# Kernel tuning notes

Measured on AMD Instinct MI355X. Metric: run time of the kernel, lower is better.

Reference implementation:

```python
import jax, jax.numpy as jnp
import numpy as np

B, C_IN, H, W = 4, 256, 200, 176
A = 6            # anchors per location (3 sizes x 2 rotations)
NUM_CLS = 4      # 3 classes + background
K = 100
N_ANCH = A * H * W


def setup_inputs() -> dict:
    key = jax.random.key(0)
    k1, k2, k3, k4, k5, k6 = jax.random.split(key, 6)
    x = jax.random.normal(k1, (B, C_IN, H, W), dtype=jnp.float32)
    scale = 1.0 / np.sqrt(C_IN)
    cls_w = jax.random.normal(k2, (NUM_CLS * A, C_IN), dtype=jnp.float32) * scale
    cls_b = jnp.zeros((NUM_CLS * A,), dtype=jnp.float32)
    reg_w = jax.random.normal(k3, (7 * A, C_IN), dtype=jnp.float32) * scale * 0.1
    reg_b = jnp.zeros((7 * A,), dtype=jnp.float32)
    # anchors: [N,7] = (x, y, z, dx, dy, dz, ry) with strictly positive sizes
    xyz = jax.random.uniform(k4, (N_ANCH, 3), minval=-35.0, maxval=35.0)
    sizes = jax.random.uniform(k5, (N_ANCH, 3), minval=1.0, maxval=4.0)
    rot = jax.random.uniform(k6, (N_ANCH, 1), minval=-np.pi, maxval=np.pi)
    anchors = jnp.concatenate([xyz, sizes, rot], axis=-1).astype(jnp.float32)
    return {"x": x, "cls_w": cls_w, "cls_b": cls_b,
            "reg_w": reg_w, "reg_b": reg_b, "anchors": anchors}


def _decode(deltas, anchors):
    # SECOND-style residual box decoder.  deltas, anchors: [B, N, 7]
    xa, ya, za, dxa, dya, dza, ra = jnp.split(anchors, 7, axis=-1)
    xt, yt, zt, dxt, dyt, dzt, rt = jnp.split(deltas, 7, axis=-1)
    diag = jnp.sqrt(dxa * dxa + dya * dya)
    xg = xt * diag + xa
    yg = yt * diag + ya
    zg = zt * dza + za
    dxg = jnp.exp(dxt) * dxa
    dyg = jnp.exp(dyt) * dya
    dzg = jnp.exp(dzt) * dza
    rg = rt + ra
    return jnp.concatenate([xg, yg, zg, dxg, dyg, dzg, rg], axis=-1)


def reference(x, cls_w, cls_b, reg_w, reg_b, anchors):
    # 1x1 conv heads: [B,C_in,H,W] -> [B,C_out,H,W]
    cls_pred = jnp.einsum('bchw,oc->bohw', x, cls_w) + cls_b[None, :, None, None]
    reg_pred = jnp.einsum('bchw,oc->bohw', x, reg_w) + reg_b[None, :, None, None]
    # permute(0,2,3,1).reshape(B, num_anchors, -1)
    cls_pred = jnp.transpose(cls_pred, (0, 2, 3, 1)).reshape(B, N_ANCH, NUM_CLS)
    reg_pred = jnp.transpose(reg_pred, (0, 2, 3, 1)).reshape(B, N_ANCH, 7)
    batch_anchors = jnp.broadcast_to(anchors[None], (B, N_ANCH, 7))
    pred_bboxes = _decode(reg_pred, batch_anchors)
    pred_scores = jax.nn.softmax(cls_pred, axis=-1)
    # per-frame top-k over max foreground score (classes 1:)
    max_scores = jnp.max(pred_scores[..., 1:], axis=-1)      # [B, N]
    _, topk_inds = jax.lax.top_k(max_scores, K)              # [B, K]
    topk_bboxes = jnp.take_along_axis(pred_bboxes, topk_inds[..., None], axis=1)
    topk_scores = jnp.take_along_axis(pred_scores, topk_inds[..., None], axis=1)
    return (topk_scores, topk_bboxes)
```

## Files before the change

### kernel.cpp

```cpp
#include <hip/hip_runtime.h>

#define BB 4
#define CIN 256
#define HW 35200
#define AA 6
#define NANCH (AA * HW)
#define TOPK 100
#define NBIN 4096
#define BINBASE 28416
#define CAP 4096
#define SMAX 4096
#define TILES 138

__device__ __forceinline__ unsigned sbin(unsigned bits) {
  int v = (int)(bits >> 15) - BINBASE;
  v = v < 0 ? 0 : v;
  v = v > (NBIN - 1) ? (NBIN - 1) : v;
  return (unsigned)v;
}

__device__ __forceinline__ float sc4(float4 l) {
  float m = fmaxf(fmaxf(l.x, l.y), fmaxf(l.z, l.w));
  float e0 = expf(l.x - m), e1 = expf(l.y - m);
  float e2 = expf(l.z - m), e3 = expf(l.w - m);
  return fmaxf(fmaxf(e1, e2), e3) / (e0 + e1 + e2 + e3);
}

#define FMA4(A, W, S)                                      \
  A.x = fmaf(S, W.x, A.x); A.y = fmaf(S, W.y, A.y);        \
  A.z = fmaf(S, W.z, A.z); A.w = fmaf(S, W.w, A.w);

__global__ __launch_bounds__(256, 4) void k1_scores(
    const float* __restrict__ x, const float* __restrict__ cls_w,
    const float* __restrict__ cls_b, unsigned int* __restrict__ hist,
    float* __restrict__ maxsc) {
  int bid = blockIdx.x;
  int b = bid / TILES, tile = bid % TILES;
  int tid = threadIdx.x;

  __shared__ __align__(16) float swf[CIN * 24];
  __shared__ unsigned lh[NBIN];
  for (int i = tid; i < CIN * 24; i += 256)
    swf[(i % CIN) * 24 + (i / CIN)] = cls_w[i];
  for (int i = tid; i < NBIN; i += 256) lh[i] = 0;
  __syncthreads();
  const float4* sw4 = (const float4*)swf;

  int hwg = tile * 256 + tid;
  bool act = hwg < HW;
  int hwc = act ? hwg : (HW - 1);
  const float* xb = x + (size_t)b * CIN * HW + hwc;

  float4 a0 = make_float4(cls_b[0], cls_b[1], cls_b[2], cls_b[3]);
  float4 a1 = make_float4(cls_b[4], cls_b[5], cls_b[6], cls_b[7]);
  float4 a2 = make_float4(cls_b[8], cls_b[9], cls_b[10], cls_b[11]);
  float4 a3 = make_float4(cls_b[12], cls_b[13], cls_b[14], cls_b[15]);
  float4 a4 = make_float4(cls_b[16], cls_b[17], cls_b[18], cls_b[19]);
  float4 a5 = make_float4(cls_b[20], cls_b[21], cls_b[22], cls_b[23]);

#pragma unroll 8
  for (int c = 0; c < CIN; ++c) {
    float xv = xb[(size_t)c * HW];
    const float4* wr = sw4 + c * 6;
    float4 w0 = wr[0], w1 = wr[1], w2 = wr[2];
    float4 w3 = wr[3], w4 = wr[4], w5 = wr[5];
    FMA4(a0, w0, xv) FMA4(a1, w1, xv) FMA4(a2, w2, xv)
    FMA4(a3, w3, xv) FMA4(a4, w4, xv) FMA4(a5, w5, xv)
  }

  if (act) {
    float s0 = sc4(a0), s1 = sc4(a1), s2 = sc4(a2);
    float s3 = sc4(a3), s4 = sc4(a4), s5 = sc4(a5);
    float* mp = maxsc + (size_t)b * NANCH + (size_t)hwg * 6u;
    mp[0] = s0; mp[1] = s1; mp[2] = s2; mp[3] = s3; mp[4] = s4; mp[5] = s5;
    atomicAdd(&lh[sbin(__float_as_uint(s0))], 1u);
    atomicAdd(&lh[sbin(__float_as_uint(s1))], 1u);
    atomicAdd(&lh[sbin(__float_as_uint(s2))], 1u);
    atomicAdd(&lh[sbin(__float_as_uint(s3))], 1u);
    atomicAdd(&lh[sbin(__float_as_uint(s4))], 1u);
    atomicAdd(&lh[sbin(__float_as_uint(s5))], 1u);
  }
  __syncthreads();
  unsigned* gh = hist + (size_t)b * NBIN;
  for (int i = tid; i < NBIN; i += 256) {
    unsigned c = lh[i];
    if (c) atomicAdd(&gh[i], c);
  }
}

__global__ __launch_bounds__(256) void k2_thresh(
    const unsigned int* __restrict__ hist, unsigned int* __restrict__ thresh) {
  int b = blockIdx.x, tid = threadIdx.x;
  const unsigned* h = hist + (size_t)b * NBIN;
  unsigned r[16];
  unsigned s = 0;
#pragma unroll
  for (int i = 0; i < 16; ++i) { r[i] = h[tid * 16 + i]; s += r[i]; }
  __shared__ unsigned seg[256];
  seg[tid] = s;
  __syncthreads();
  for (int d = 1; d < 256; d <<= 1) {
    unsigned add = (tid + d < 256) ? seg[tid + d] : 0u;
    __syncthreads();
    seg[tid] += add;
    __syncthreads();
  }
  unsigned above = (tid < 255) ? seg[tid + 1] : 0u;
  if (above < TOPK && above + s >= TOPK) {
    unsigned c = above, T = 0;
    for (int i = 15; i >= 0; --i) {
      c += r[i];
      if (c >= TOPK) { T = tid * 16u + (unsigned)i; break; }
    }
    thresh[b] = T;
  }
}

__global__ __launch_bounds__(256) void k3_compact(
    const float* __restrict__ maxsc, const unsigned int* __restrict__ thresh,
    unsigned int* __restrict__ cand_count, unsigned long long* __restrict__ cand) {
  unsigned p = blockIdx.x * 256u + threadIdx.x;
  unsigned b = p / NANCH, n = p % NANCH;
  unsigned bits = __float_as_uint(maxsc[p]);
  bool pred = sbin(bits) >= thresh[b];
  unsigned long long mask = __ballot(pred);
  if (mask) {
    int lane = threadIdx.x & 63;
    int leader = (int)__ffsll((unsigned long long)mask) - 1;
    unsigned base = 0;
    if (lane == leader)
      base = atomicAdd(&cand_count[b], (unsigned)__popcll(mask));
    base = __shfl(base, leader, 64);
    if (pred) {
      unsigned pos = base + (unsigned)__popcll(mask & ((1ull << lane) - 1ull));
      if (pos < CAP)
        cand[(size_t)b * CAP + pos] =
            ((unsigned long long)bits << 32) | (unsigned)(~n);
    }
  }
}

__global__ __launch_bounds__(256) void k4_sort(
    const unsigned long long* __restrict__ cand,
    const unsigned int* __restrict__ cand_count, unsigned int* __restrict__ topk) {
  int b = blockIdx.x, tid = threadIdx.x;
  __shared__ unsigned long long sh[SMAX];
  unsigned cnt = cand_count[b];
  if (cnt > CAP) cnt = CAP;
  unsigned S = 128;
  while (S < cnt) S <<= 1;
  for (unsigned t = tid; t < S; t += 256)
    sh[t] = (t < cnt) ? cand[(size_t)b * CAP + t] : 0ULL;
  __syncthreads();
  for (unsigned kk = 2; kk <= S; kk <<= 1) {
    for (unsigned jj = kk >> 1; jj > 0; jj >>= 1) {
      for (unsigned t = tid; t < S; t += 256) {
        unsigned ixj = t ^ jj;
        if (ixj > t) {
          unsigned long long a = sh[t], c = sh[ixj];
          bool sw = ((t & kk) == 0) ? (a < c) : (a > c);
          if (sw) { sh[t] = c; sh[ixj] = a; }
        }
      }
      __syncthreads();
    }
  }
  if (tid < TOPK)
    topk[b * TOPK + tid] = ~(unsigned)(sh[tid] & 0xFFFFFFFFULL);
}

__global__ __launch_bounds__(256) void k5_out(
    const float* __restrict__ x, const float* __restrict__ cls_w,
    const float* __restrict__ cls_b, const float* __restrict__ reg_w,
    const float* __restrict__ reg_b, const float* __restrict__ anchors,
    const unsigned int* __restrict__ topk, float* __restrict__ out) {
  int bk = blockIdx.x;
  int b = bk / TOPK, k = bk % TOPK;
  unsigned n = topk[b * TOPK + k];
  int a = (int)(n % AA);
  unsigned hw = n / AA;
  int tid = threadIdx.x;

  float xv = x[(size_t)b * CIN * HW + (size_t)tid * HW + hw];
  float part[11];
#pragma unroll
  for (int j = 0; j < 4; ++j) part[j] = xv * cls_w[(a * 4 + j) * CIN + tid];
#pragma unroll
  for (int j = 0; j < 7; ++j) part[4 + j] = xv * reg_w[(a * 7 + j) * CIN + tid];

#pragma unroll
  for (int j = 0; j < 11; ++j) {
    float v = part[j];
    for (int off = 32; off > 0; off >>= 1) v += __shfl_down(v, off, 64);
    part[j] = v;
  }
  __shared__ float red[4][11];
  int wave = tid >> 6, lane = tid & 63;
  if (lane == 0) {
#pragma unroll
    for (int j = 0; j < 11; ++j) red[wave][j] = part[j];
  }
  __syncthreads();
  if (tid == 0) {
    float tot[11];
#pragma unroll
    for (int j = 0; j < 11; ++j)
      tot[j] = red[0][j] + red[1][j] + red[2][j] + red[3][j];
    float l0 = tot[0] + cls_b[a * 4 + 0];
    float l1 = tot[1] + cls_b[a * 4 + 1];
    float l2 = tot[2] + cls_b[a * 4 + 2];
    float l3 = tot[3] + cls_b[a * 4 + 3];
    float m = fmaxf(fmaxf(l0, l1), fmaxf(l2, l3));
    float e0 = expf(l0 - m), e1 = expf(l1 - m);
    float e2 = expf(l2 - m), e3 = expf(l3 - m);
    float inv = 1.0f / (e0 + e1 + e2 + e3);
    float* os = out + ((size_t)b * TOPK + k) * 4;
    os[0] = e0 * inv; os[1] = e1 * inv; os[2] = e2 * inv; os[3] = e3 * inv;
    const float* an = anchors + (size_t)n * 7;
    float xa = an[0], ya = an[1], za = an[2];
    float dxa = an[3], dya = an[4], dza = an[5], ra = an[6];
    float xt = tot[4] + reg_b[a * 7 + 0];
    float yt = tot[5] + reg_b[a * 7 + 1];
    float zt = tot[6] + reg_b[a * 7 + 2];
    float dxt = tot[7] + reg_b[a * 7 + 3];
    float dyt = tot[8] + reg_b[a * 7 + 4];
    float dzt = tot[9] + reg_b[a * 7 + 5];
    float rt = tot[10] + reg_b[a * 7 + 6];
    float diag = sqrtf(dxa * dxa + dya * dya);
    float* ob = out + (size_t)BB * TOPK * 4 + ((size_t)b * TOPK + k) * 7;
    ob[0] = xt * diag + xa;
    ob[1] = yt * diag + ya;
    ob[2] = zt * dza + za;
    ob[3] = expf(dxt) * dxa;
    ob[4] = expf(dyt) * dya;
    ob[5] = expf(dzt) * dza;
    ob[6] = rt + ra;
  }
}

extern "C" void kernel_launch(void* const* d_in, const int* in_sizes, int n_in,
                              void* d_out, int out_size, void* d_ws, size_t ws_size,
                              hipStream_t stream) {
  const float* x       = (const float*)d_in[0];
  const float* cls_w   = (const float*)d_in[1];
  const float* cls_b   = (const float*)d_in[2];
  const float* reg_w   = (const float*)d_in[3];
  const float* reg_b   = (const float*)d_in[4];
  const float* anchors = (const float*)d_in[5];
  float* out = (float*)d_out;

  char* ws = (char*)d_ws;
  size_t off = 0;
  unsigned int* hist = (unsigned int*)(ws + off);        off += (size_t)BB * NBIN * 4;
  unsigned int* cand_count = (unsigned int*)(ws + off);  off += 64;
  unsigned int* thresh = (unsigned int*)(ws + off);      off += 64;
  unsigned long long* cand = (unsigned long long*)(ws + off); off += (size_t)BB * CAP * 8;
  unsigned int* topk = (unsigned int*)(ws + off);        off += 2048;
  float* maxsc = (float*)(ws + off);

  hipMemsetAsync(hist, 0, (size_t)BB * NBIN * 4 + 64, stream);

  k1_scores<<<BB * TILES, 256, 0, stream>>>(x, cls_w, cls_b, hist, maxsc);
  k2_thresh<<<BB, 256, 0, stream>>>(hist, thresh);
  k3_compact<<<(BB * NANCH) / 256, 256, 0, stream>>>(maxsc, thresh, cand_count, cand);
  k4_sort<<<BB, 256, 0, stream>>>(cand, cand_count, topk);
  k5_out<<<BB * TOPK, 256, 0, stream>>>(x, cls_w, cls_b, reg_w, reg_b, anchors,
                                        topk, out);
}
```

Before: 277.7 us.

## Fold threshold and sort into last-block tails, pre-transpose weights in init kernel

Replaces the memset and the separate threshold and sort kernels with last-block-done patterns: the final tile of each batch in the score kernel computes the histogram threshold, and the final block per batch in the compaction kernel runs the bitonic sort. A new init kernel zeroes the counters and writes the transposed cls weights to global memory once, so the score kernel reads weights from global or cache instead of staging them in LDS, and its unroll drops from 8 to 4. This removes two launches and a memset but adds atomic counters, fences, and a large shared sort buffer allocated in every compaction block, which can hurt that kernel's occupancy.

```diff
diff --git a/kernel.cpp b/kernel.cpp
--- a/kernel.cpp
+++ b/kernel.cpp
@@ -11,6 +11,10 @@
 #define CAP 4096
 #define SMAX 4096
 #define TILES 138
+#define ZEROWORDS (BB * NBIN + 48)
+
+#define ALOAD_U32(p) __hip_atomic_load((p), __ATOMIC_RELAXED, __HIP_MEMORY_SCOPE_AGENT)
+#define ALOAD_U64(p) __hip_atomic_load((p), __ATOMIC_RELAXED, __HIP_MEMORY_SCOPE_AGENT)
 
 __device__ __forceinline__ unsigned sbin(unsigned bits) {
   int v = (int)(bits >> 15) - BINBASE;
@@ -30,21 +34,30 @@
   A.x = fmaf(S, W.x, A.x); A.y = fmaf(S, W.y, A.y);        \
   A.z = fmaf(S, W.z, A.z); A.w = fmaf(S, W.w, A.w);
 
+__global__ __launch_bounds__(256) void k0_init(
+    const float* __restrict__ cls_w, float* __restrict__ wt,
+    unsigned int* __restrict__ zr) {
+  int t = blockIdx.x * 256 + threadIdx.x;
+  int stride = gridDim.x * 256;
+  for (int i = t; i < ZEROWORDS; i += stride) zr[i] = 0u;
+  for (int i = t; i < 24 * CIN; i += stride)
+    wt[(i % CIN) * 24 + (i / CIN)] = cls_w[i];
+}
+
 __global__ __launch_bounds__(256, 4) void k1_scores(
-    const float* __restrict__ x, const float* __restrict__ cls_w,
+    const float* __restrict__ x, const float* __restrict__ wt,
     const float* __restrict__ cls_b, unsigned int* __restrict__ hist,
-    float* __restrict__ maxsc) {
+    float* __restrict__ maxsc, unsigned int* __restrict__ done1,
+    unsigned int* __restrict__ thresh) {
   int bid = blockIdx.x;
   int b = bid / TILES, tile = bid % TILES;
   int tid = threadIdx.x;
 
-  __shared__ __align__(16) float swf[CIN * 24];
   __shared__ unsigned lh[NBIN];
-  for (int i = tid; i < CIN * 24; i += 256)
-    swf[(i % CIN) * 24 + (i / CIN)] = cls_w[i];
+  __shared__ unsigned seg[256];
+  __shared__ unsigned lastf;
   for (int i = tid; i < NBIN; i += 256) lh[i] = 0;
   __syncthreads();
-  const float4* sw4 = (const float4*)swf;
 
   int hwg = tile * 256 + tid;
   bool act = hwg < HW;
@@ -58,10 +71,10 @@
   float4 a4 = make_float4(cls_b[16], cls_b[17], cls_b[18], cls_b[19]);
   float4 a5 = make_float4(cls_b[20], cls_b[21], cls_b[22], cls_b[23]);
 
-#pragma unroll 8
+#pragma unroll 4
   for (int c = 0; c < CIN; ++c) {
     float xv = xb[(size_t)c * HW];
-    const float4* wr = sw4 + c * 6;
+    const float4* wr = (const float4*)(wt + c * 24);
     float4 w0 = wr[0], w1 = wr[1], w2 = wr[2];
     float4 w3 = wr[3], w4 = wr[4], w5 = wr[5];
     FMA4(a0, w0, xv) FMA4(a1, w1, xv) FMA4(a2, w2, xv)
@@ -86,39 +99,47 @@
     unsigned c = lh[i];
     if (c) atomicAdd(&gh[i], c);
   }
-}
-
-__global__ __launch_bounds__(256) void k2_thresh(
-    const unsigned int* __restrict__ hist, unsigned int* __restrict__ thresh) {
-  int b = blockIdx.x, tid = threadIdx.x;
-  const unsigned* h = hist + (size_t)b * NBIN;
-  unsigned r[16];
-  unsigned s = 0;
-#pragma unroll
-  for (int i = 0; i < 16; ++i) { r[i] = h[tid * 16 + i]; s += r[i]; }
-  __shared__ unsigned seg[256];
-  seg[tid] = s;
-  __syncthreads();
-  for (int d = 1; d < 256; d <<= 1) {
-    unsigned add = (tid + d < 256) ? seg[tid + d] : 0u;
+  __syncthreads();
+  if (tid == 0) {
+    __threadfence();
+    lastf = (atomicAdd(&done1[b], 1u) == TILES - 1) ? 1u : 0u;
+  }
+  __syncthreads();
+  if (lastf) {
+    __threadfence();
+    unsigned r[16];
+    unsigned s = 0;
+#pragma unroll
+    for (int i = 0; i < 16; ++i) {
+      r[i] = ALOAD_U32(&gh[tid * 16 + i]);
+      s += r[i];
+    }
+    seg[tid] = s;
     __syncthreads();
-    seg[tid] += add;
-    __syncthreads();
-  }
-  unsigned above = (tid < 255) ? seg[tid + 1] : 0u;
-  if (above < TOPK && above + s >= TOPK) {
-    unsigned c = above, T = 0;
-    for (int i = 15; i >= 0; --i) {
-      c += r[i];
-      if (c >= TOPK) { T = tid * 16u + (unsigned)i; break; }
-    }
-    thresh[b] = T;
+    for (int d = 1; d < 256; d <<= 1) {
+      unsigned add = (tid + d < 256) ? seg[tid + d] : 0u;
+      __syncthreads();
+      seg[tid] += add;
+      __syncthreads();
+    }
+    unsigned above = (tid < 255) ? seg[tid + 1] : 0u;
+    if (above < TOPK && above + s >= TOPK) {
+      unsigned cc = above, T = 0;
+      for (int i = 15; i >= 0; --i) {
+        cc += r[i];
+        if (cc >= TOPK) { T = tid * 16u + (unsigned)i; break; }
+      }
+      thresh[b] = T;
+    }
   }
 }
 
 __global__ __launch_bounds__(256) void k3_compact(
     const float* __restrict__ maxsc, const unsigned int* __restrict__ thresh,
-    unsigned int* __restrict__ cand_count, unsigned long long* __restrict__ cand) {
+    unsigned int* __restrict__ cand_count, unsigned long long* __restrict__ cand,
+    unsigned int* __restrict__ done2, unsigned int* __restrict__ topk) {
+  __shared__ unsigned long long sh[SMAX];
+  __shared__ unsigned lastf;
   unsigned p = blockIdx.x * 256u + threadIdx.x;
   unsigned b = p / NANCH, n = p % NANCH;
   unsigned bits = __float_as_uint(maxsc[p]);
@@ -126,7 +147,7 @@
   unsigned long long mask = __ballot(pred);
   if (mask) {
     int lane = threadIdx.x & 63;
-    int leader = (int)__ffsll((unsigned long long)mask) - 1;
+    int leader = (int)__ffsll(mask) - 1;
     unsigned base = 0;
     if (lane == leader)
       base = atomicAdd(&cand_count[b], (unsigned)__popcll(mask));
@@ -134,23 +155,25 @@
     if (pred) {
       unsigned pos = base + (unsigned)__popcll(mask & ((1ull << lane) - 1ull));
       if (pos < CAP)
-        cand[(size_t)b * CAP + pos] =
-            ((unsigned long long)bits << 32) | (unsigned)(~n);
-    }
-  }
-}
-
-__global__ __launch_bounds__(256) void k4_sort(
-    const unsigned long long* __restrict__ cand,
-    const unsigned int* __restrict__ cand_count, unsigned int* __restrict__ topk) {
-  int b = blockIdx.x, tid = threadIdx.x;
-  __shared__ unsigned long long sh[SMAX];
-  unsigned cnt = cand_count[b];
+        atomicExch(&cand[(size_t)b * CAP + pos],
+                   ((unsigned long long)bits << 32) | (unsigned)(~n));
+    }
+  }
+  __syncthreads();
+  if (threadIdx.x == 0) {
+    __threadfence();
+    lastf = (atomicAdd(&done2[b], 1u) == (NANCH / 256u) - 1u) ? 1u : 0u;
+  }
+  __syncthreads();
+  if (!lastf) return;
+  __threadfence();
+  int tid = threadIdx.x;
+  unsigned cnt = ALOAD_U32(&cand_count[b]);
   if (cnt > CAP) cnt = CAP;
   unsigned S = 128;
   while (S < cnt) S <<= 1;
   for (unsigned t = tid; t < S; t += 256)
-    sh[t] = (t < cnt) ? cand[(size_t)b * CAP + t] : 0ULL;
+    sh[t] = (t < cnt) ? ALOAD_U64(&cand[(size_t)b * CAP + t]) : 0ULL;
   __syncthreads();
   for (unsigned kk = 2; kk <= S; kk <<= 1) {
     for (unsigned jj = kk >> 1; jj > 0; jj >>= 1) {
@@ -250,20 +273,20 @@
   float* out = (float*)d_out;
 
   char* ws = (char*)d_ws;
-  size_t off = 0;
-  unsigned int* hist = (unsigned int*)(ws + off);        off += (size_t)BB * NBIN * 4;
-  unsigned int* cand_count = (unsigned int*)(ws + off);  off += 64;
-  unsigned int* thresh = (unsigned int*)(ws + off);      off += 64;
-  unsigned long long* cand = (unsigned long long*)(ws + off); off += (size_t)BB * CAP * 8;
-  unsigned int* topk = (unsigned int*)(ws + off);        off += 2048;
-  float* maxsc = (float*)(ws + off);
-
-  hipMemsetAsync(hist, 0, (size_t)BB * NBIN * 4 + 64, stream);
-
-  k1_scores<<<BB * TILES, 256, 0, stream>>>(x, cls_w, cls_b, hist, maxsc);
-  k2_thresh<<<BB, 256, 0, stream>>>(hist, thresh);
-  k3_compact<<<(BB * NANCH) / 256, 256, 0, stream>>>(maxsc, thresh, cand_count, cand);
-  k4_sort<<<BB, 256, 0, stream>>>(cand, cand_count, topk);
+  unsigned int* hist       = (unsigned int*)(ws);
+  unsigned int* cand_count = (unsigned int*)(ws + 65536);
+  unsigned int* done1      = (unsigned int*)(ws + 65600);
+  unsigned int* done2      = (unsigned int*)(ws + 65664);
+  unsigned int* thresh     = (unsigned int*)(ws + 65728);
+  unsigned int* topk       = (unsigned int*)(ws + 65792);
+  float* wt                = (float*)(ws + 67840);
+  unsigned long long* cand = (unsigned long long*)(ws + 92416);
+  float* maxsc             = (float*)(ws + 223488);
+
+  k0_init<<<80, 256, 0, stream>>>(cls_w, wt, hist);
+  k1_scores<<<BB * TILES, 256, 0, stream>>>(x, wt, cls_b, hist, maxsc, done1, thresh);
+  k3_compact<<<(BB * NANCH) / 256, 256, 0, stream>>>(maxsc, thresh, cand_count, cand,
+                                                     done2, topk);
   k5_out<<<BB * TOPK, 256, 0, stream>>>(x, cls_w, cls_b, reg_w, reg_b, anchors,
                                         topk, out);
 }
```

Result: slower. 379.1 us (+36.5%).
